# Optimization experiments

Hardware: AMD Instinct MI355X
Metric: run time of the kernel (lower is better)

Reference implementation:

```python
import jax, jax.numpy as jnp
import numpy as np

LN_EPS = 1e-5
NORM_EPS = 1e-12
TEMPERATURE = 0.5


def _project(h, W1, b1, W2, b2, g, beta):
    # projection head: Linear -> ReLU -> Linear -> LayerNorm, then L2 normalize
    x = jnp.maximum(h @ W1 + b1, 0.0) @ W2 + b2          # [B, P]
    mu = jnp.mean(x, axis=-1, keepdims=True)
    var = jnp.mean(jnp.square(x - mu), axis=-1, keepdims=True)
    x = (x - mu) * jax.lax.rsqrt(var + LN_EPS) * g + beta
    n = jnp.linalg.norm(x, axis=-1, keepdims=True)
    return x / jnp.maximum(n, NORM_EPS)                   # [B, P]


def setup_inputs() -> dict:
    key = jax.random.key(0)
    ks = jax.random.split(key, 8)
    B, H, P, K, NBUF = 16384, 2048, 256, 64, 2000
    Hh = H // 2
    return {
        "hidden_states": jax.random.normal(ks[0], (B, H), jnp.float32),
        "positive_hidden": jax.random.normal(ks[1], (B, H), jnp.float32),
        "neg_buffer": jax.random.normal(ks[2], (NBUF, P), jnp.float32),
        "W1": jax.random.normal(ks[3], (H, Hh), jnp.float32) * (1.0 / np.sqrt(H)),
        "b1": jnp.zeros((Hh,), jnp.float32),
        "W2": jax.random.normal(ks[4], (Hh, P), jnp.float32) * (1.0 / np.sqrt(Hh)),
        "b2": jnp.zeros((P,), jnp.float32),
        "ln_gamma": jnp.ones((P,), jnp.float32),
        "ln_beta": jnp.zeros((P,), jnp.float32),
        "neg_indices": jax.random.randint(ks[5], (B, K), 0, NBUF, jnp.int32),
    }


def reference(hidden_states, positive_hidden, neg_buffer, W1, b1, W2, b2,
              ln_gamma, ln_beta, neg_indices):
    anchors = _project(hidden_states, W1, b1, W2, b2, ln_gamma, ln_beta)      # [B,P]
    positives = _project(positive_hidden, W1, b1, W2, b2, ln_gamma, ln_beta)  # [B,P]
    # negatives are detached in the original (buffer stores .detach() features)
    negs = jax.lax.stop_gradient(neg_buffer)[neg_indices]                      # [B,K,P]
    pos_sim = jnp.einsum('bp,bp->b', anchors, positives) / TEMPERATURE        # [B]
    neg_sims = jnp.einsum('bkp,bp->bk', negs, anchors) / TEMPERATURE          # [B,K]
    logits = jnp.concatenate([pos_sim[:, None], neg_sims], axis=1)            # [B,1+K]
    # cross-entropy with label 0 for every anchor, averaged over the batch
    loss = -jnp.mean(jax.nn.log_softmax(logits, axis=-1)[:, 0])
    return loss
```

## Files before the change

### kernel.cpp

```cpp
#include <hip/hip_runtime.h>
#include <hip/hip_bf16.h>
#include <cstdint>

#define BATCH   16384
#define HDIM    2048
#define HHDIM   1024
#define PDIM    256
#define KNEG    64
#define NBUF    2000
#define M1      (2 * BATCH)

typedef float  f32x4  __attribute__((ext_vector_type(4)));
typedef __bf16 bf16x8 __attribute__((ext_vector_type(8)));

typedef __attribute__((address_space(3))) unsigned int       lds_u32;
typedef __attribute__((address_space(1))) const unsigned int glb_u32;

__device__ __forceinline__ void gload_lds16(const void* g, void* l) {
  __builtin_amdgcn_global_load_lds((glb_u32*)g, (lds_u32*)l, 16, 0, 0);
}

__device__ __forceinline__ float dot4(f32x4 a, f32x4 b) {
  return a[0]*b[0] + a[1]*b[1] + a[2]*b[2] + a[3]*b[3];
}

#define VMCNT(n) asm volatile("s_waitcnt vmcnt(" #n ")" ::: "memory")
#define LGKM(n)  asm volatile("s_waitcnt lgkmcnt(" #n ")" ::: "memory")

__global__ __launch_bounds__(256)
void cast_bf16_kernel(const float* __restrict__ src, __bf16* __restrict__ dst,
                      long n8) {
  long i = (long)blockIdx.x * blockDim.x + threadIdx.x;
  long stride = (long)gridDim.x * blockDim.x;
  for (; i < n8; i += stride) {
    f32x4 a = ((const f32x4*)src)[2 * i];
    f32x4 b = ((const f32x4*)src)[2 * i + 1];
    bf16x8 w;
    for (int j = 0; j < 4; ++j) { w[j] = (__bf16)a[j]; w[4 + j] = (__bf16)b[j]; }
    ((bf16x8*)dst)[i] = w;
  }
}

__global__ void transpose_cast_kernel(const float* __restrict__ src,
                                      __bf16* __restrict__ dst, int K, int N) {
  __shared__ float tile[32][33];
  int bn = blockIdx.x * 32, bk = blockIdx.y * 32;
  int tx = threadIdx.x, ty = threadIdx.y;
  for (int j = 0; j < 32; j += 8)
    tile[ty + j][tx] = src[(size_t)(bk + ty + j) * N + bn + tx];
  __syncthreads();
  for (int j = 0; j < 32; j += 8)
    dst[(size_t)(bn + ty + j) * K + bk + tx] = (__bf16)tile[tx][ty + j];
}

template <int KD, int BMH, int NBt, bool RELU_OUT, bool LNFUSE, int GRID>
__global__ __launch_bounds__(512)
void gemm_8ph(const __bf16* __restrict__ A, const __bf16* __restrict__ Bt,
              const float* __restrict__ bias,
              const float* __restrict__ lng, const float* __restrict__ lnb,
              void* __restrict__ Cv) {
  static_assert(!LNFUSE || NBt == 1, "LN fusion needs full rows per block");
  constexpr int KT    = KD / 64;
  constexpr int MI    = BMH / 32;
  constexpr int AHALF = BMH * 64;
  constexpr int BHALF = 128 * 64;
  constexpr int ASTEP = 2 * AHALF;
  constexpr int BSTEP = 2 * BHALF;
  constexpr int NDIM  = NBt * 256;
  constexpr int AUL   = BMH / 64;

  __shared__ __bf16 lA[2 * ASTEP];
  __shared__ __bf16 lB[2 * BSTEP];

  constexpr int Q = GRID / 8;
  int bid = blockIdx.x;
  int swb = (bid & 7) * Q + (bid >> 3);
  const int mb = swb / NBt, nb = swb % NBt;
  const long mrow0 = (long)mb * (2 * BMH);
  const int  ncol0 = nb * 256;

  const int tid = threadIdx.x;
  const int wid = tid >> 6, lane = tid & 63;
  const int wr = wid >> 2, wc = wid & 3;
  const int fl = lane & 15, fh = lane >> 4;

  int aoff[MI][2], boff[2][2];
  #pragma unroll
  for (int mi = 0; mi < MI; ++mi)
    #pragma unroll
    for (int ks = 0; ks < 2; ++ks) {
      int row = wr * (BMH / 2) + mi * 16 + fl;
      aoff[mi][ks] = row * 64 + (((ks * 4 + fh) ^ (row & 7)) * 8);
    }
  #pragma unroll
  for (int ni = 0; ni < 2; ++ni)
    #pragma unroll
    for (int ks = 0; ks < 2; ++ks) {
      int row = wc * 32 + ni * 16 + fl;
      boff[ni][ks] = row * 64 + (((ks * 4 + fh) ^ (row & 7)) * 8);
    }

  const int r0 = tid >> 3, sl = tid & 7;
  long aS[2][AUL], bS[2][2];
  #pragma unroll
  for (int h = 0; h < 2; ++h) {
    #pragma unroll
    for (int i = 0; i < AUL; ++i) {
      int rr = r0 + i * 64;
      int ss = sl ^ (rr & 7);
      aS[h][i] = (mrow0 + h * BMH + rr) * (long)KD + ss * 8;
    }
    #pragma unroll
    for (int i = 0; i < 2; ++i) {
      int rr = r0 + i * 64;
      int ss = sl ^ (rr & 7);
      bS[h][i] = ((long)(ncol0 + h * 128 + rr)) * KD + ss * 8;
    }
  }
  const int dstw = wid * 512;

  auto stA = [&](int h, int t) {
    __bf16* base = lA + (t & 1) * ASTEP + h * AHALF + dstw;
    #pragma unroll
    for (int i = 0; i < AUL; ++i)
      gload_lds16(A + aS[h][i] + (long)t * 64, (void*)(base + i * 4096));
  };
  auto stB = [&](int h, int t) {
    __bf16* base = lB + (t & 1) * BSTEP + h * BHALF + dstw;
    #pragma unroll
    for (int i = 0; i < 2; ++i)
      gload_lds16(Bt + bS[h][i] + (long)t * 64, (void*)(base + i * 4096));
  };

  bf16x8 areg[MI][2], breg0[2][2], breg1[2][2];
  auto loadA = [&](int mh, int s) {
    const __bf16* base = lA + (s & 1) * ASTEP + mh * AHALF;
    #pragma unroll
    for (int mi = 0; mi < MI; ++mi)
      #pragma unroll
      for (int ks = 0; ks < 2; ++ks)
        areg[mi][ks] = *(const bf16x8*)(base + aoff[mi][ks]);
  };
  auto loadB = [&](bf16x8 (&br)[2][2], int nh, int s) {
    const __bf16* base = lB + (s & 1) * BSTEP + nh * BHALF;
    #pragma unroll
    for (int ni = 0; ni < 2; ++ni)
      #pragma unroll
      for (int ks = 0; ks < 2; ++ks)
        br[ni][ks] = *(const bf16x8*)(base + boff[ni][ks]);
  };

  f32x4 acc[2][2][MI][2] = {};

#define PHASE_MFMA(mh, nh, BR)                                                \
  __builtin_amdgcn_s_setprio(1);                                              \
  _Pragma("unroll")                                                           \
  for (int ks = 0; ks < 2; ++ks) {                                            \
    _Pragma("unroll")                                                         \
    for (int mi = 0; mi < MI; ++mi) {                                         \
      _Pragma("unroll")                                                       \
      for (int ni = 0; ni < 2; ++ni)                                          \
        acc[mh][nh][mi][ni] = __builtin_amdgcn_mfma_f32_16x16x32_bf16(        \
            areg[mi][ks], BR[ni][ks], acc[mh][nh][mi][ni], 0, 0, 0);          \
    }                                                                         \
  }                                                                           \
  __builtin_amdgcn_s_setprio(0);

  stA(0, 0); stB(0, 0); stA(1, 0); stB(1, 0);
  stA(0, 1); stB(1, 1); stB(0, 1); stA(1, 1);
  if constexpr (BMH == 128) { VMCNT(8); } else { VMCNT(6); }
  __builtin_amdgcn_s_barrier();
  __builtin_amdgcn_sched_barrier(0);

  for (int s = 0; s < KT; ++s) {
    loadA(0, s);
    loadB(breg0, 0, s);
    if (s >= 1 && s + 1 < KT) stB(0, s + 1);
    if constexpr (BMH == 128) LGKM(8);
    __builtin_amdgcn_s_barrier();
    LGKM(0);
    __builtin_amdgcn_sched_barrier(0);
    PHASE_MFMA(0, 0, breg0);
    __builtin_amdgcn_s_barrier();

    loadB(breg1, 1, s);
    if (s >= 1 && s + 1 < KT) stA(1, s + 1);
    __builtin_amdgcn_s_barrier();
    LGKM(0);
    __builtin_amdgcn_sched_barrier(0);
    PHASE_MFMA(0, 1, breg1);
    __builtin_amdgcn_s_barrier();

    loadA(1, s);
    if (s + 2 < KT) stA(0, s + 2);
    __builtin_amdgcn_s_barrier();
    LGKM(0);
    __builtin_amdgcn_sched_barrier(0);
    PHASE_MFMA(1, 1, breg1);
    __builtin_amdgcn_s_barrier();

    if (s + 2 < KT) stB(1, s + 2);
    __builtin_amdgcn_s_barrier();
    __builtin_amdgcn_sched_barrier(0);
    PHASE_MFMA(1, 0, breg0);
    if (s + 2 < KT) {
      if constexpr (BMH == 128) { VMCNT(4); } else { VMCNT(3); }
    } else {
      VMCNT(0);
    }
    __builtin_amdgcn_s_barrier();
    __builtin_amdgcn_sched_barrier(0);
  }

#undef PHASE_MFMA

  if constexpr (LNFUSE) {
    float (*s1p)[4] = (float(*)[4])((float*)lA);
    float (*s2p)[4] = (float(*)[4])((float*)lA + 512);
    float (*n2p)[4] = (float(*)[4])((float*)lA + 1024);

    float v[2][2][MI][2][4];
    float gg[2][2], bb[2][2];
    #pragma unroll
    for (int nh = 0; nh < 2; ++nh)
      #pragma unroll
      for (int ni = 0; ni < 2; ++ni) {
        int c = nh * 128 + wc * 32 + ni * 16 + fl;
        float bv = bias[c];
        gg[nh][ni] = lng[c]; bb[nh][ni] = lnb[c];
        #pragma unroll
        for (int mh = 0; mh < 2; ++mh)
          #pragma unroll
          for (int mi = 0; mi < MI; ++mi)
            #pragma unroll
            for (int r = 0; r < 4; ++r)
              v[mh][nh][mi][ni][r] = acc[mh][nh][mi][ni][r] + bv;
      }

    #pragma unroll
    for (int mh = 0; mh < 2; ++mh)
      #pragma unroll
      for (int mi = 0; mi < MI; ++mi)
        #pragma unroll
        for (int r = 0; r < 4; ++r) {
          float s1 = 0.0f, s2 = 0.0f;
          #pragma unroll
          for (int nh = 0; nh < 2; ++nh)
            #pragma unroll
            for (int ni = 0; ni < 2; ++ni) {
              float x = v[mh][nh][mi][ni][r];
              s1 += x; s2 += x * x;
            }
          for (int m = 1; m < 16; m <<= 1) {
            s1 += __shfl_xor(s1, m, 64);
            s2 += __shfl_xor(s2, m, 64);
          }
          if (fl == 0) {
            int lr = mh * 64 + wr * 32 + mi * 16 + fh * 4 + r;
            s1p[lr][wc] = s1; s2p[lr][wc] = s2;
          }
        }
    __syncthreads();

    float n2loc[2][MI][4];
    #pragma unroll
    for (int mh = 0; mh < 2; ++mh)
      #pragma unroll
      for (int mi = 0; mi < MI; ++mi)
        #pragma unroll
        for (int r = 0; r < 4; ++r) {
          int lr = mh * 64 + wr * 32 + mi * 16 + fh * 4 + r;
          float t1 = s1p[lr][0] + s1p[lr][1] + s1p[lr][2] + s1p[lr][3];
          float t2 = s2p[lr][0] + s2p[lr][1] + s2p[lr][2] + s2p[lr][3];
          float mu = t1 * (1.0f / PDIM);
          float var = t2 * (1.0f / PDIM) - mu * mu;
          float rstd = rsqrtf(var + 1e-5f);
          float n2 = 0.0f;
          #pragma unroll
          for (int nh = 0; nh < 2; ++nh)
            #pragma unroll
            for (int ni = 0; ni < 2; ++ni) {
              float y = (v[mh][nh][mi][ni][r] - mu) * rstd * gg[nh][ni] + bb[nh][ni];
              v[mh][nh][mi][ni][r] = y;
              n2 += y * y;
            }
          for (int m = 1; m < 16; m <<= 1) n2 += __shfl_xor(n2, m, 64);
          n2loc[mh][mi][r] = n2;
        }
    #pragma unroll
    for (int mh = 0; mh < 2; ++mh)
      #pragma unroll
      for (int mi = 0; mi < MI; ++mi)
        #pragma unroll
        for (int r = 0; r < 4; ++r)
          if (fl == 0) {
            int lr = mh * 64 + wr * 32 + mi * 16 + fh * 4 + r;
            n2p[lr][wc] = n2loc[mh][mi][r];
          }
    __syncthreads();

    #pragma unroll
    for (int mh = 0; mh < 2; ++mh)
      #pragma unroll
      for (int mi = 0; mi < MI; ++mi)
        #pragma unroll
        for (int r = 0; r < 4; ++r) {
          int lr = mh * 64 + wr * 32 + mi * 16 + fh * 4 + r;
          float t = n2p[lr][0] + n2p[lr][1] + n2p[lr][2] + n2p[lr][3];
          float sc = 1.0f / fmaxf(sqrtf(t), 1e-12f);
          #pragma unroll
          for (int nh = 0; nh < 2; ++nh)
            #pragma unroll
            for (int ni = 0; ni < 2; ++ni) {
              int c = nh * 128 + wc * 32 + ni * 16 + fl;
              ((float*)Cv)[(mrow0 + lr) * NDIM + c] = v[mh][nh][mi][ni][r] * sc;
            }
        }
  } else {
    #pragma unroll
    for (int mh = 0; mh < 2; ++mh)
      #pragma unroll
      for (int nh = 0; nh < 2; ++nh)
        #pragma unroll
        for (int ni = 0; ni < 2; ++ni) {
          int col = ncol0 + nh * 128 + wc * 32 + ni * 16 + fl;
          float bv = bias[col];
          #pragma unroll
          for (int mi = 0; mi < MI; ++mi)
            #pragma unroll
            for (int r = 0; r < 4; ++r) {
              long row = mrow0 + mh * BMH + wr * (BMH / 2) + mi * 16 + fh * 4 + r;
              float x = acc[mh][nh][mi][ni][r] + bv;
              if constexpr (RELU_OUT) {
                x = fmaxf(x, 0.0f);
                ((__bf16*)Cv)[row * NDIM + col] = (__bf16)x;
              } else {
                ((float*)Cv)[row * NDIM + col] = x;
              }
            }
        }
  }
}

__global__ __launch_bounds__(256)
void loss_kernel(const float* __restrict__ X, const __bf16* __restrict__ negb,
                 const int* __restrict__ nidx, float* __restrict__ partials) {
  __shared__ float lsum[4];
  int b    = blockIdx.x * 4 + (threadIdx.x >> 6);
  int lane = threadIdx.x & 63;
  int g = lane >> 4, lg = lane & 15;

  const float* arow = X + (size_t)b * PDIM;
  const float* prow = X + (size_t)(BATCH + b) * PDIM;

  float a16[16];
  #pragma unroll
  for (int j = 0; j < 4; ++j) {
    f32x4 av = *(const f32x4*)(arow + lg * 16 + j * 4);
    #pragma unroll
    for (int e = 0; e < 4; ++e) a16[j * 4 + e] = av[e];
  }

  float ps = 0.0f;
  #pragma unroll
  for (int j = 0; j < 4; ++j) {
    f32x4 p = *(const f32x4*)(prow + lg * 16 + j * 4);
    #pragma unroll
    for (int e = 0; e < 4; ++e) ps += a16[j * 4 + e] * p[e];
  }
  for (int m = 1; m < 16; m <<= 1) ps += __shfl_xor(ps, m, 64);
  float pos = ps * 2.0f;

  float myneg = -3.0e38f;
  for (int k4 = 0; k4 < 16; ++k4) {
    int k = k4 * 4 + g;
    int idx = nidx[(size_t)b * KNEG + k];
    const __bf16* nrow = negb + (size_t)idx * PDIM;
    float sv = 0.0f;
    #pragma unroll
    for (int j = 0; j < 2; ++j) {
      bf16x8 nv = *(const bf16x8*)(nrow + lg * 16 + j * 8);
      #pragma unroll
      for (int e = 0; e < 8; ++e) sv += a16[j * 8 + e] * (float)nv[e];
    }
    for (int m = 1; m < 16; m <<= 1) sv += __shfl_xor(sv, m, 64);
    if (lg == k4) myneg = sv * 2.0f;
  }

  float mx = myneg;
  for (int m = 1; m < 64; m <<= 1) mx = fmaxf(mx, __shfl_xor(mx, m, 64));
  mx = fmaxf(mx, pos);
  float e = expf(myneg - mx);
  for (int m = 1; m < 64; m <<= 1) e += __shfl_xor(e, m, 64);
  float tot = e + expf(pos - mx);
  float lb = -(pos - mx - logf(tot));

  if (lane == 0) lsum[threadIdx.x >> 6] = lb;
  __syncthreads();
  if (threadIdx.x == 0)
    partials[blockIdx.x] = lsum[0] + lsum[1] + lsum[2] + lsum[3];
}

__global__ void finalize_kernel(const float* __restrict__ partials,
                                float* __restrict__ out) {
  __shared__ float ls[4];
  int tid = threadIdx.x;
  float s = 0.0f;
  for (int i = tid; i < 4096; i += 256) s += partials[i];
  for (int m = 1; m < 64; m <<= 1) s += __shfl_xor(s, m, 64);
  if ((tid & 63) == 0) ls[tid >> 6] = s;
  __syncthreads();
  if (tid == 0) out[0] = (ls[0] + ls[1] + ls[2] + ls[3]) * (1.0f / BATCH);
}

extern "C" void kernel_launch(void* const* d_in, const int* in_sizes, int n_in,
                              void* d_out, int out_size, void* d_ws, size_t ws_size,
                              hipStream_t stream) {
  const float* hidden   = (const float*)d_in[0];
  const float* positive = (const float*)d_in[1];
  const float* negbuf   = (const float*)d_in[2];
  const float* W1       = (const float*)d_in[3];
  const float* b1       = (const float*)d_in[4];
  const float* W2       = (const float*)d_in[5];
  const float* b2       = (const float*)d_in[6];
  const float* gamma    = (const float*)d_in[7];
  const float* beta     = (const float*)d_in[8];
  const int*   nidx     = (const int*)d_in[9];
  float* out = (float*)d_out;

  char* ws = (char*)d_ws;
  const size_t OFF_Y1   = 134217728;
  const size_t OFF_W1T  = OFF_Y1 + 67108864;
  const size_t OFF_W2T  = OFF_W1T + 4194304;
  const size_t OFF_NEGB = OFF_W2T + 524288;
  const size_t OFF_PART = OFF_NEGB + 1048576;

  __bf16* Abf      = (__bf16*)(ws);
  __bf16* Y1       = (__bf16*)(ws + OFF_Y1);
  __bf16* W1T      = (__bf16*)(ws + OFF_W1T);
  __bf16* W2T      = (__bf16*)(ws + OFF_W2T);
  __bf16* negb     = (__bf16*)(ws + OFF_NEGB);
  float*  partials = (float*) (ws + OFF_PART);
  float*  X        = (float*) (ws);

  transpose_cast_kernel<<<dim3(HHDIM / 32, HDIM / 32), dim3(32, 8), 0, stream>>>(
      W1, W1T, HDIM, HHDIM);
  transpose_cast_kernel<<<dim3(PDIM / 32, HHDIM / 32), dim3(32, 8), 0, stream>>>(
      W2, W2T, HHDIM, PDIM);

  const long n8 = (long)BATCH * HDIM / 8;
  cast_bf16_kernel<<<2048, 256, 0, stream>>>(hidden, Abf, n8);
  cast_bf16_kernel<<<2048, 256, 0, stream>>>(positive, Abf + (size_t)BATCH * HDIM, n8);
  cast_bf16_kernel<<<256, 256, 0, stream>>>(negbuf, negb, (long)NBUF * PDIM / 8);

  gemm_8ph<HDIM, 128, HHDIM / 256, true, false, (M1 / 256) * (HHDIM / 256)>
      <<<(M1 / 256) * (HHDIM / 256), 512, 0, stream>>>(
          Abf, W1T, b1, nullptr, nullptr, Y1);

  gemm_8ph<HHDIM, 64, PDIM / 256, false, true, (M1 / 128) * (PDIM / 256)>
      <<<(M1 / 128) * (PDIM / 256), 512, 0, stream>>>(
          Y1, W2T, b2, gamma, beta, X);

  loss_kernel<<<BATCH / 4, 256, 0, stream>>>(X, negb, nidx, partials);
  finalize_kernel<<<1, 256, 0, stream>>>(partials, out);
}
```

Baseline: 303.2 us.

## Double-buffer A fragments in registers and overlap LDS reads with MFMA phases

Rewrites the GEMM main loop schedule so the A fragments use two register sets, and the LDS reads for the next phase or next k-step are issued before or alongside the current MFMA phase. This removes the per-phase LGKM waits and extra barriers. The cost is more register pressure and retuned vmcnt waits, which could lower occupancy or expose LDS hazards if the counts are wrong.

```diff
diff --git a/kernel.cpp b/kernel.cpp
--- a/kernel.cpp
+++ b/kernel.cpp
@@ -20,12 +20,7 @@
   __builtin_amdgcn_global_load_lds((glb_u32*)g, (lds_u32*)l, 16, 0, 0);
 }
 
-__device__ __forceinline__ float dot4(f32x4 a, f32x4 b) {
-  return a[0]*b[0] + a[1]*b[1] + a[2]*b[2] + a[3]*b[3];
-}
-
 #define VMCNT(n) asm volatile("s_waitcnt vmcnt(" #n ")" ::: "memory")
-#define LGKM(n)  asm volatile("s_waitcnt lgkmcnt(" #n ")" ::: "memory")
 
 __global__ __launch_bounds__(256)
 void cast_bf16_kernel(const float* __restrict__ src, __bf16* __restrict__ dst,
@@ -132,14 +127,14 @@
       gload_lds16(Bt + bS[h][i] + (long)t * 64, (void*)(base + i * 4096));
   };
 
-  bf16x8 areg[MI][2], breg0[2][2], breg1[2][2];
-  auto loadA = [&](int mh, int s) {
+  bf16x8 aregA[MI][2], aregB[MI][2], breg0[2][2], breg1[2][2];
+  auto loadA = [&](bf16x8 (&ar)[MI][2], int mh, int s) {
     const __bf16* base = lA + (s & 1) * ASTEP + mh * AHALF;
     #pragma unroll
     for (int mi = 0; mi < MI; ++mi)
       #pragma unroll
       for (int ks = 0; ks < 2; ++ks)
-        areg[mi][ks] = *(const bf16x8*)(base + aoff[mi][ks]);
+        ar[mi][ks] = *(const bf16x8*)(base + aoff[mi][ks]);
   };
   auto loadB = [&](bf16x8 (&br)[2][2], int nh, int s) {
     const __bf16* base = lB + (s & 1) * BSTEP + nh * BHALF;
@@ -152,7 +147,7 @@
 
   f32x4 acc[2][2][MI][2] = {};
 
-#define PHASE_MFMA(mh, nh, BR)                                                \
+#define PHASE_MFMA(mh, nh, AR, BR)                                            \
   __builtin_amdgcn_s_setprio(1);                                              \
   _Pragma("unroll")                                                           \
   for (int ks = 0; ks < 2; ++ks) {                                            \
@@ -161,52 +156,54 @@
       _Pragma("unroll")                                                       \
       for (int ni = 0; ni < 2; ++ni)                                          \
         acc[mh][nh][mi][ni] = __builtin_amdgcn_mfma_f32_16x16x32_bf16(        \
-            areg[mi][ks], BR[ni][ks], acc[mh][nh][mi][ni], 0, 0, 0);          \
+            AR[mi][ks], BR[ni][ks], acc[mh][nh][mi][ni], 0, 0, 0);            \
     }                                                                         \
   }                                                                           \
   __builtin_amdgcn_s_setprio(0);
 
   stA(0, 0); stB(0, 0); stA(1, 0); stB(1, 0);
   stA(0, 1); stB(1, 1); stB(0, 1); stA(1, 1);
-  if constexpr (BMH == 128) { VMCNT(8); } else { VMCNT(6); }
+  if constexpr (AUL == 2) { VMCNT(8); } else { VMCNT(6); }
   __builtin_amdgcn_s_barrier();
   __builtin_amdgcn_sched_barrier(0);
+  loadA(aregA, 0, 0);
+  loadB(breg0, 0, 0);
 
   for (int s = 0; s < KT; ++s) {
-    loadA(0, s);
-    loadB(breg0, 0, s);
     if (s >= 1 && s + 1 < KT) stB(0, s + 1);
-    if constexpr (BMH == 128) LGKM(8);
-    __builtin_amdgcn_s_barrier();
-    LGKM(0);
-    __builtin_amdgcn_sched_barrier(0);
-    PHASE_MFMA(0, 0, breg0);
-    __builtin_amdgcn_s_barrier();
-
     loadB(breg1, 1, s);
-    if (s >= 1 && s + 1 < KT) stA(1, s + 1);
-    __builtin_amdgcn_s_barrier();
-    LGKM(0);
-    __builtin_amdgcn_sched_barrier(0);
-    PHASE_MFMA(0, 1, breg1);
-    __builtin_amdgcn_s_barrier();
-
-    loadA(1, s);
-    if (s + 2 < KT) stA(0, s + 2);
-    __builtin_amdgcn_s_barrier();
-    LGKM(0);
-    __builtin_amdgcn_sched_barrier(0);
-    PHASE_MFMA(1, 1, breg1);
-    __builtin_amdgcn_s_barrier();
-
-    if (s + 2 < KT) stB(1, s + 2);
+    PHASE_MFMA(0, 0, aregA, breg0);
+    if (s + 1 < KT) {
+      if constexpr (AUL == 2) { VMCNT(6); } else { VMCNT(5); }
+    } else {
+      VMCNT(0);
+    }
     __builtin_amdgcn_s_barrier();
     __builtin_amdgcn_sched_barrier(0);
-    PHASE_MFMA(1, 0, breg0);
+
+    if (s >= 1 && s + 1 < KT) stA(1, s + 1);
+    loadA(aregB, 1, s);
+    PHASE_MFMA(0, 1, aregA, breg1);
+    __builtin_amdgcn_s_barrier();
+    __builtin_amdgcn_sched_barrier(0);
+
+    if (s + 2 < KT) stA(0, s + 2);
+    PHASE_MFMA(1, 1, aregB, breg1);
     if (s + 2 < KT) {
-      if constexpr (BMH == 128) { VMCNT(4); } else { VMCNT(3); }
+      if constexpr (AUL == 2) { VMCNT(4); } else { VMCNT(2); }
+    } else if (s + 1 < KT) {
+      if constexpr (AUL == 2) { VMCNT(2); } else { VMCNT(1); }
     } else {
       VMCNT(0);
+    }
+    __builtin_amdgcn_s_barrier();
+    __builtin_amdgcn_sched_barrier(0);
+
+    if (s + 2 < KT) stB(1, s + 2);
+    PHASE_MFMA(1, 0, aregB, breg0);
+    if (s + 1 < KT) {
+      loadA(aregA, 0, s + 1);
+      loadB(breg0, 0, s + 1);
     }
     __builtin_amdgcn_s_barrier();
     __builtin_amdgcn_sched_barrier(0);
```

Measured after the change: 304.3 us. Within noise of the previous version (+0.4%).
